# Performance work log

Measured on AMD Instinct MI355X. Metric: run time of the kernel, lower is better.

Reference implementation:

```python
import jax, jax.numpy as jnp
import numpy as np

N_HEADS = 8
D_EMBED = 512
D_HEAD = D_EMBED // N_HEADS  # used only for the scale factor, as in the source


def setup_inputs() -> dict:
    key = jax.random.key(0)
    k1, k2, k3, k4, k5 = jax.random.split(key, 5)
    B, S, D = 4, 4096, D_EMBED
    s = 1.0 / np.sqrt(D)
    return {
        "x": jax.random.normal(k1, (B, S, D), dtype=jnp.float32),
        "w_in": jax.random.normal(k2, (3 * D, D), dtype=jnp.float32) * s,
        "b_in": jax.random.normal(k3, (3 * D,), dtype=jnp.float32) * 0.01,
        "w_out": jax.random.normal(k4, (D, D), dtype=jnp.float32) * s,
        "b_out": jax.random.normal(k5, (D,), dtype=jnp.float32) * 0.01,
    }


def reference(x, w_in, b_in, w_out, b_out):
    # in_proj: torch Linear y = x @ W.T + b ; chunk into q,k,v along last dim
    qkv = jnp.einsum("bsd,ed->bse", x, w_in) + b_in  # [B,S,3D]
    q, k, v = jnp.split(qkv, 3, axis=-1)  # each [B,S,D]
    # NOTE: source never splits into heads; attention over full d_embed,
    # but scaled by sqrt(d_head) = sqrt(d_embed / n_heads).
    scores = jnp.einsum("bqd,bkd->bqk", q, k) / np.sqrt(D_HEAD)  # [B,S,S]
    weight = jax.nn.softmax(scores, axis=-1)
    out = jnp.einsum("bqk,bkd->bqd", weight, v)  # [B,S,D]
    out = jnp.einsum("bsd,ed->bse", out, w_out) + b_out
    return out
```

## Files before the change

kernel.cpp:

```cpp
#include <hip/hip_runtime.h>

typedef __bf16 bf16x8 __attribute__((ext_vector_type(8)));
typedef float f32x4 __attribute__((ext_vector_type(4)));

#define MFMA16(a, b, c) __builtin_amdgcn_mfma_f32_16x16x32_bf16(a, b, c, 0, 0, 0)
#define LOG2E 1.44269504088896340736f

__device__ __forceinline__ unsigned short f2bf(float f) {
  union { float f; unsigned u; } v; v.f = f;
  return (unsigned short)((v.u + 0x7fffu + ((v.u >> 16) & 1u)) >> 16);
}
__device__ __forceinline__ bf16x8 ld_frag(const unsigned short* p) {
  return *(const bf16x8*)p;
}
__device__ __forceinline__ void gld_lds16(const unsigned short* g, unsigned short* l) {
  __builtin_amdgcn_global_load_lds(
      (const __attribute__((address_space(1))) unsigned int*)(const void*)g,
      (__attribute__((address_space(3))) unsigned int*)(void*)l, 16, 0, 0);
}

__global__ void cvt_f2bf(const float* __restrict__ in,
                         unsigned short* __restrict__ out, int n4) {
  int i = blockIdx.x * blockDim.x + threadIdx.x;
  if (i < n4) {
    float4 v = ((const float4*)in)[i];
    ushort4 o;
    o.x = f2bf(v.x); o.y = f2bf(v.y); o.z = f2bf(v.z); o.w = f2bf(v.w);
    ((ushort4*)out)[i] = o;
  }
}

__global__ void gemm_bt(const unsigned short* __restrict__ A,
                        const unsigned short* __restrict__ B,
                        const float* __restrict__ bias,
                        float* __restrict__ outf,
                        unsigned short* __restrict__ qbuf,
                        unsigned short* __restrict__ kbuf,
                        unsigned short* __restrict__ vtbuf,
                        int M, int N, int K, int mode) {
  __shared__ alignas(16) unsigned short As[128 * 32];
  __shared__ alignas(16) unsigned short Bs[128 * 32];
  const int n0 = blockIdx.x * 128, m0 = blockIdx.y * 128;
  const int tid = threadIdx.x;
  const int l = tid & 63, w = tid >> 6;
  const int quad = l >> 4, c = l & 15;
  const int wm = (w >> 1) * 64, wn = (w & 1) * 64;

  f32x4 acc[4][4] = {};
  const int kiters = K >> 5;
  for (int kt = 0; kt < kiters; ++kt) {
    __syncthreads();
    const int kk = kt * 32 + (l & 3) * 8;
    const int row = l >> 2;
#pragma unroll
    for (int i = 0; i < 2; ++i) {
      const int rbase = i * 64 + w * 16;
      gld_lds16(&A[(size_t)(m0 + rbase + row) * K + kk], &As[rbase * 32]);
      gld_lds16(&B[(size_t)(n0 + rbase + row) * K + kk], &Bs[rbase * 32]);
    }
    __syncthreads();
    bf16x8 af[4], bfr[4];
#pragma unroll
    for (int t = 0; t < 4; ++t) {
      af[t] = ld_frag(&As[(wm + t * 16 + c) * 32 + quad * 8]);
      bfr[t] = ld_frag(&Bs[(wn + t * 16 + c) * 32 + quad * 8]);
    }
#pragma unroll
    for (int mt = 0; mt < 4; ++mt)
#pragma unroll
      for (int nt = 0; nt < 4; ++nt)
        acc[mt][nt] = MFMA16(af[mt], bfr[nt], acc[mt][nt]);
  }

#pragma unroll
  for (int nt = 0; nt < 4; ++nt) {
    const int n = n0 + wn + nt * 16 + c;
    const float bsum = bias[n];
#pragma unroll
    for (int mt = 0; mt < 4; ++mt) {
      const int mbase = m0 + wm + mt * 16 + quad * 4;
      if (mode == 0) {
#pragma unroll
        for (int r = 0; r < 4; ++r)
          outf[(size_t)(mbase + r) * N + n] = acc[mt][nt][r] + bsum;
      } else if (n < 1024) {
        unsigned short* dst = (n < 512) ? qbuf : kbuf;
        const int nn = n & 511;
#pragma unroll
        for (int r = 0; r < 4; ++r)
          dst[(size_t)(mbase + r) * 512 + nn] = f2bf(acc[mt][nt][r] + bsum);
      } else {
        const int d = n - 1024;
        const int bb = mbase >> 12, s = mbase & 4095;
        ushort4 pk;
        pk.x = f2bf(acc[mt][nt][0] + bsum);
        pk.y = f2bf(acc[mt][nt][1] + bsum);
        pk.z = f2bf(acc[mt][nt][2] + bsum);
        pk.w = f2bf(acc[mt][nt][3] + bsum);
        *(ushort4*)&vtbuf[((size_t)bb * 512 + d) * 4096 + s] = pk;
      }
    }
  }
}

#define KROW 520
#define PROW 40

__global__ __launch_bounds__(256, 1) void attn_kernel(
    const unsigned short* __restrict__ Q, const unsigned short* __restrict__ Kb,
    const unsigned short* __restrict__ Vt, unsigned short* __restrict__ O) {
  __shared__ alignas(16) unsigned short k_lds[2][32 * KROW];
  __shared__ alignas(16) unsigned short v_lds[2][512 * 32];
  __shared__ alignas(16) unsigned short p_lds[4 * 16 * PROW];

  const int bid = blockIdx.x;
  const int xcd = bid & 7;
  const int b = xcd >> 1;
  const int qt = (bid >> 3) | ((xcd & 1) << 5);
  const int s0 = qt * 64;
  const int tid = threadIdx.x;
  const int l = tid & 63, w = tid >> 6;
  const int quad = l >> 4, c = l & 15;
  const size_t boff = (size_t)b * 4096 * 512;

  bf16x8 qf[16];
  {
    const unsigned short* qrow = Q + boff + (size_t)(s0 + w * 16 + c) * 512;
#pragma unroll
    for (int ks = 0; ks < 16; ++ks) qf[ks] = ld_frag(&qrow[ks * 32 + quad * 8]);
  }

  f32x4 o[32] = {};
  float m_run = -1e30f, l_run = 0.f;

  const unsigned short* Kbase = Kb + boff;
  const unsigned short* Vbase = Vt + (size_t)b * 512 * 4096;

  auto stage = [&](int buf, int kv0) {
#pragma unroll
    for (int i = 0; i < 8; ++i) {
      const int row = i * 4 + w;
      gld_lds16(&Kbase[(size_t)(kv0 + row) * 512 + l * 8], &k_lds[buf][row * KROW]);
    }
#pragma unroll
    for (int i = 0; i < 8; ++i) {
      const int dbase = (i * 4 + w) * 16;
      const int d = dbase + (l >> 2);
      const int jl = (l & 3) ^ ((d >> 1) & 3);
      gld_lds16(&Vbase[(size_t)d * 4096 + kv0 + jl * 8], &v_lds[buf][dbase * 32]);
    }
  };

  stage(0, 0);
  for (int it = 0; it < 128; ++it) {
    const int buf = it & 1;
    __syncthreads();
    if (it + 1 < 128) stage(buf ^ 1, (it + 1) * 32);

    f32x4 sa[2][2] = {};
#pragma unroll
    for (int ks = 0; ks < 16; ++ks) {
      const unsigned short* kr = &k_lds[buf][c * KROW + ks * 32 + quad * 8];
      bf16x8 kf0 = ld_frag(kr);
      bf16x8 kf1 = ld_frag(kr + 16 * KROW);
      sa[0][ks & 1] = MFMA16(kf0, qf[ks], sa[0][ks & 1]);
      sa[1][ks & 1] = MFMA16(kf1, qf[ks], sa[1][ks & 1]);
    }
    const f32x4 s0v = sa[0][0] + sa[0][1];
    const f32x4 s1v = sa[1][0] + sa[1][1];

    const float C1 = 0.125f * LOG2E;
    float m8 = fmaxf(fmaxf(fmaxf(s0v[0], s0v[1]), fmaxf(s0v[2], s0v[3])),
                     fmaxf(fmaxf(s1v[0], s1v[1]), fmaxf(s1v[2], s1v[3])));
    m8 = fmaxf(m8, __shfl_xor(m8, 16));
    m8 = fmaxf(m8, __shfl_xor(m8, 32));
    const float mn = fmaxf(m_run, m8);

    float p0[4], p1[4], s8 = 0.f;
#pragma unroll
    for (int r = 0; r < 4; ++r) {
      p0[r] = exp2f((s0v[r] - mn) * C1);
      p1[r] = exp2f((s1v[r] - mn) * C1);
      s8 += p0[r] + p1[r];
    }
    unsigned short* prow = &p_lds[(w * 16 + c) * PROW];
    ushort4 pk0, pk1;
    pk0.x = f2bf(p0[0]); pk0.y = f2bf(p0[1]); pk0.z = f2bf(p0[2]); pk0.w = f2bf(p0[3]);
    pk1.x = f2bf(p1[0]); pk1.y = f2bf(p1[1]); pk1.z = f2bf(p1[2]); pk1.w = f2bf(p1[3]);
    *(ushort4*)&prow[quad * 4] = pk0;
    *(ushort4*)&prow[16 + quad * 4] = pk1;

    s8 += __shfl_xor(s8, 16);
    s8 += __shfl_xor(s8, 32);

    if (__any(mn > m_run)) {
      const float alpha = exp2f((m_run - mn) * C1);
      l_run = l_run * alpha + s8;
      m_run = mn;
#pragma unroll
      for (int t = 0; t < 32; ++t) o[t] *= alpha;
    } else {
      l_run += s8;
    }

    asm volatile("s_waitcnt lgkmcnt(0)" ::: "memory");

    const bf16x8 pf = ld_frag(&p_lds[(w * 16 + c) * PROW + quad * 8]);
#pragma unroll
    for (int t = 0; t < 32; ++t) {
      const int d = t * 16 + c;
      const int jp = quad ^ ((d >> 1) & 3);
      bf16x8 vf = ld_frag(&v_lds[buf][d * 32 + jp * 8]);
      o[t] = MFMA16(vf, pf, o[t]);
    }
  }

  const float inv = 1.0f / l_run;
  unsigned short* orow = O + boff + (size_t)(s0 + w * 16 + c) * 512;
#pragma unroll
  for (int t = 0; t < 32; ++t) {
    ushort4 pk;
    pk.x = f2bf(o[t][0] * inv);
    pk.y = f2bf(o[t][1] * inv);
    pk.z = f2bf(o[t][2] * inv);
    pk.w = f2bf(o[t][3] * inv);
    *(ushort4*)&orow[t * 16 + quad * 4] = pk;
  }
}

extern "C" void kernel_launch(void* const* d_in, const int* in_sizes, int n_in,
                              void* d_out, int out_size, void* d_ws, size_t ws_size,
                              hipStream_t stream) {
  const float* x = (const float*)d_in[0];
  const float* w_in = (const float*)d_in[1];
  const float* b_in = (const float*)d_in[2];
  const float* w_out = (const float*)d_in[3];
  const float* b_out = (const float*)d_in[4];
  float* out = (float*)d_out;

  const size_t MTOT = (size_t)4 * 4096 * 512;
  unsigned short* q = (unsigned short*)d_ws;
  unsigned short* k = q + MTOT;
  unsigned short* vt = k + MTOT;
  unsigned short* xbf_ao = vt + MTOT;
  unsigned short* w_in_bf = xbf_ao + MTOT;
  unsigned short* w_out_bf = w_in_bf + 1536 * 512;

  cvt_f2bf<<<dim3((int)(MTOT / 4 / 256)), 256, 0, stream>>>(x, xbf_ao,
                                                            (int)(MTOT / 4));
  cvt_f2bf<<<dim3(768), 256, 0, stream>>>(w_in, w_in_bf, 1536 * 512 / 4);
  cvt_f2bf<<<dim3(256), 256, 0, stream>>>(w_out, w_out_bf, 512 * 512 / 4);

  gemm_bt<<<dim3(12, 128), 256, 0, stream>>>(xbf_ao, w_in_bf, b_in, nullptr, q,
                                             k, vt, 16384, 1536, 512, 1);
  attn_kernel<<<dim3(256), 256, 0, stream>>>(q, k, vt, xbf_ao);
  gemm_bt<<<dim3(4, 128), 256, 0, stream>>>(xbf_ao, w_out_bf, b_out, out,
                                            nullptr, nullptr, nullptr, 16384,
                                            512, 512, 0);
}
```

Measured before the change: 443.1 us.

## Split attention KV range into two halves with merge kernel for more parallelism

Splits the key/value sequence into two halves so the attention kernel launches twice as many blocks, each writing a normalized partial output plus per-row max and sum. A new merge kernel combines the two partials with log-sum-exp weights. LDS double buffering is dropped to single buffers with two barriers per iteration so two blocks can fit per CU. The cost is an extra kernel, a second partial buffer, bf16 rounding of the partials, and no overlap between loads and compute inside a block.

```diff
diff --git a/kernel.cpp b/kernel.cpp
--- a/kernel.cpp
+++ b/kernel.cpp
@@ -106,18 +106,21 @@
 #define KROW 520
 #define PROW 40
 
-__global__ __launch_bounds__(256, 1) void attn_kernel(
+__global__ __launch_bounds__(256, 2) void attn_kernel(
     const unsigned short* __restrict__ Q, const unsigned short* __restrict__ Kb,
-    const unsigned short* __restrict__ Vt, unsigned short* __restrict__ O) {
-  __shared__ alignas(16) unsigned short k_lds[2][32 * KROW];
-  __shared__ alignas(16) unsigned short v_lds[2][512 * 32];
+    const unsigned short* __restrict__ Vt, unsigned short* __restrict__ part0,
+    unsigned short* __restrict__ part1, float2* __restrict__ mlbuf) {
+  __shared__ alignas(16) unsigned short k_lds[32 * KROW];
+  __shared__ alignas(16) unsigned short v_lds[512 * 32];
   __shared__ alignas(16) unsigned short p_lds[4 * 16 * PROW];
 
   const int bid = blockIdx.x;
   const int xcd = bid & 7;
   const int b = xcd >> 1;
-  const int qt = (bid >> 3) | ((xcd & 1) << 5);
+  const int half = (bid >> 3) & 1;
+  const int qt = (bid >> 4) | ((xcd & 1) << 5);
   const int s0 = qt * 64;
+  const int kvbase = half * 2048;
   const int tid = threadIdx.x;
   const int l = tid & 63, w = tid >> 6;
   const int quad = l >> 4, c = l & 15;
@@ -136,31 +139,30 @@
   const unsigned short* Kbase = Kb + boff;
   const unsigned short* Vbase = Vt + (size_t)b * 512 * 4096;
 
-  auto stage = [&](int buf, int kv0) {
+  auto stage = [&](int kv0) {
 #pragma unroll
     for (int i = 0; i < 8; ++i) {
       const int row = i * 4 + w;
-      gld_lds16(&Kbase[(size_t)(kv0 + row) * 512 + l * 8], &k_lds[buf][row * KROW]);
+      gld_lds16(&Kbase[(size_t)(kv0 + row) * 512 + l * 8], &k_lds[row * KROW]);
     }
 #pragma unroll
     for (int i = 0; i < 8; ++i) {
       const int dbase = (i * 4 + w) * 16;
       const int d = dbase + (l >> 2);
       const int jl = (l & 3) ^ ((d >> 1) & 3);
-      gld_lds16(&Vbase[(size_t)d * 4096 + kv0 + jl * 8], &v_lds[buf][dbase * 32]);
+      gld_lds16(&Vbase[(size_t)d * 4096 + kv0 + jl * 8], &v_lds[dbase * 32]);
     }
   };
 
-  stage(0, 0);
-  for (int it = 0; it < 128; ++it) {
-    const int buf = it & 1;
-    __syncthreads();
-    if (it + 1 < 128) stage(buf ^ 1, (it + 1) * 32);
+  for (int it = 0; it < 64; ++it) {
+    __syncthreads();
+    stage(kvbase + it * 32);
+    __syncthreads();
 
     f32x4 sa[2][2] = {};
 #pragma unroll
     for (int ks = 0; ks < 16; ++ks) {
-      const unsigned short* kr = &k_lds[buf][c * KROW + ks * 32 + quad * 8];
+      const unsigned short* kr = &k_lds[c * KROW + ks * 32 + quad * 8];
       bf16x8 kf0 = ld_frag(kr);
       bf16x8 kf1 = ld_frag(kr + 16 * KROW);
       sa[0][ks & 1] = MFMA16(kf0, qf[ks], sa[0][ks & 1]);
@@ -210,13 +212,14 @@
     for (int t = 0; t < 32; ++t) {
       const int d = t * 16 + c;
       const int jp = quad ^ ((d >> 1) & 3);
-      bf16x8 vf = ld_frag(&v_lds[buf][d * 32 + jp * 8]);
+      bf16x8 vf = ld_frag(&v_lds[d * 32 + jp * 8]);
       o[t] = MFMA16(vf, pf, o[t]);
     }
   }
 
+  unsigned short* part = half ? part1 : part0;
   const float inv = 1.0f / l_run;
-  unsigned short* orow = O + boff + (size_t)(s0 + w * 16 + c) * 512;
+  unsigned short* orow = part + boff + (size_t)(s0 + w * 16 + c) * 512;
 #pragma unroll
   for (int t = 0; t < 32; ++t) {
     ushort4 pk;
@@ -226,6 +229,38 @@
     pk.w = f2bf(o[t][3] * inv);
     *(ushort4*)&orow[t * 16 + quad * 4] = pk;
   }
+  if (quad == 0) {
+    float2 ml; ml.x = m_run; ml.y = l_run;
+    mlbuf[(size_t)half * 16384 + b * 4096 + s0 + w * 16 + c] = ml;
+  }
+}
+
+__global__ void merge_halves(const unsigned short* __restrict__ p1,
+                             const float2* __restrict__ mlbuf,
+                             unsigned short* __restrict__ p0out) {
+  const int i = blockIdx.x * blockDim.x + threadIdx.x;
+  const int row = i >> 6;
+  const float2 a = mlbuf[row];
+  const float2 bb = mlbuf[16384 + row];
+  const float C1 = 0.125f * LOG2E;
+  const float M = fmaxf(a.x, bb.x);
+  float w0 = a.y * exp2f((a.x - M) * C1);
+  float w1 = bb.y * exp2f((bb.x - M) * C1);
+  const float inv = 1.0f / (w0 + w1);
+  w0 *= inv; w1 *= inv;
+  bf16x8 v0 = *(const bf16x8*)(p0out + (size_t)i * 8);
+  bf16x8 v1 = *(const bf16x8*)(p1 + (size_t)i * 8);
+  ushort4 o0, o1;
+  o0.x = f2bf(w0 * (float)v0[0] + w1 * (float)v1[0]);
+  o0.y = f2bf(w0 * (float)v0[1] + w1 * (float)v1[1]);
+  o0.z = f2bf(w0 * (float)v0[2] + w1 * (float)v1[2]);
+  o0.w = f2bf(w0 * (float)v0[3] + w1 * (float)v1[3]);
+  o1.x = f2bf(w0 * (float)v0[4] + w1 * (float)v1[4]);
+  o1.y = f2bf(w0 * (float)v0[5] + w1 * (float)v1[5]);
+  o1.z = f2bf(w0 * (float)v0[6] + w1 * (float)v1[6]);
+  o1.w = f2bf(w0 * (float)v0[7] + w1 * (float)v1[7]);
+  *(ushort4*)(p0out + (size_t)i * 8) = o0;
+  *(ushort4*)(p0out + (size_t)i * 8 + 4) = o1;
 }
 
 extern "C" void kernel_launch(void* const* d_in, const int* in_sizes, int n_in,
@@ -242,19 +277,22 @@
   unsigned short* q = (unsigned short*)d_ws;
   unsigned short* k = q + MTOT;
   unsigned short* vt = k + MTOT;
-  unsigned short* xbf_ao = vt + MTOT;
-  unsigned short* w_in_bf = xbf_ao + MTOT;
+  unsigned short* xbf = vt + MTOT;
+  unsigned short* part1 = xbf + MTOT;
+  unsigned short* w_in_bf = part1 + MTOT;
   unsigned short* w_out_bf = w_in_bf + 1536 * 512;
-
-  cvt_f2bf<<<dim3((int)(MTOT / 4 / 256)), 256, 0, stream>>>(x, xbf_ao,
+  float2* mlbuf = (float2*)(w_out_bf + 512 * 512);
+
+  cvt_f2bf<<<dim3((int)(MTOT / 4 / 256)), 256, 0, stream>>>(x, xbf,
                                                             (int)(MTOT / 4));
   cvt_f2bf<<<dim3(768), 256, 0, stream>>>(w_in, w_in_bf, 1536 * 512 / 4);
   cvt_f2bf<<<dim3(256), 256, 0, stream>>>(w_out, w_out_bf, 512 * 512 / 4);
 
-  gemm_bt<<<dim3(12, 128), 256, 0, stream>>>(xbf_ao, w_in_bf, b_in, nullptr, q,
-                                             k, vt, 16384, 1536, 512, 1);
-  attn_kernel<<<dim3(256), 256, 0, stream>>>(q, k, vt, xbf_ao);
-  gemm_bt<<<dim3(4, 128), 256, 0, stream>>>(xbf_ao, w_out_bf, b_out, out,
-                                            nullptr, nullptr, nullptr, 16384,
-                                            512, 512, 0);
-}
+  gemm_bt<<<dim3(12, 128), 256, 0, stream>>>(xbf, w_in_bf, b_in, nullptr, q, k,
+                                             vt, 16384, 1536, 512, 1);
+  attn_kernel<<<dim3(512), 256, 0, stream>>>(q, k, vt, xbf, part1, mlbuf);
+  merge_halves<<<dim3(4096), 256, 0, stream>>>(part1, mlbuf, xbf);
+  gemm_bt<<<dim3(4, 128), 256, 0, stream>>>(xbf, w_out_bf, b_out, out, nullptr,
+                                            nullptr, nullptr, 16384, 512, 512,
+                                            0);
+}
```

New measurement: 432.3 us. -2.4%, faster.
